# Performance work log

Measured on AMD Instinct MI355X. Metric: run time of the kernel, lower is better.

Reference implementation:

```python
import jax, jax.numpy as jnp
import numpy as np

N = 50000      # nodes
E = 800000     # edges
G = 1024       # graphs in batch
D_IN = 9       # atom feature dim
D = 64         # embedding_size


def _lin(k, fan_in, shape):
    s = 1.0 / np.sqrt(fan_in)
    return jax.random.uniform(k, shape, jnp.float32, -s, s)


def setup_inputs() -> dict:
    key = jax.random.key(0)
    ks = jax.random.split(key, 12)
    x = jax.random.normal(ks[0], (N, D_IN), dtype=jnp.float32)
    edge_index = jax.random.randint(ks[1], (2, E), 0, N, dtype=jnp.int32)
    # node -> graph id, sorted, every graph non-empty
    batch = (jnp.arange(N) * G // N).astype(jnp.int32)
    W0 = _lin(ks[2], D_IN, (D_IN, D)); b0 = _lin(ks[3], D_IN, (D,))
    W1 = _lin(ks[4], D, (D, D));       b1 = _lin(ks[5], D, (D,))
    W2 = _lin(ks[6], D, (D, D));       b2 = _lin(ks[7], D, (D,))
    W3 = _lin(ks[8], D, (D, D));       b3 = _lin(ks[9], D, (D,))
    Wout = _lin(ks[10], 2 * D, (2 * D, 1)); bout = _lin(ks[11], 2 * D, (1,))
    return {"x": x, "edge_index": edge_index, "batch": batch,
            "W0": W0, "b0": b0, "W1": W1, "b1": b1,
            "W2": W2, "b2": b2, "W3": W3, "b3": b3,
            "Wout": Wout, "bout": bout}


def reference(x, edge_index, batch, W0, b0, W1, b1, W2, b2, W3, b3, Wout, bout):
    n = x.shape[0]
    # GCNConv: add self-loops, symmetric normalization D^-1/2 (A+I) D^-1/2
    loops = jnp.arange(n, dtype=edge_index.dtype)
    row = jnp.concatenate([edge_index[0], loops])  # source
    col = jnp.concatenate([edge_index[1], loops])  # destination
    deg = jax.ops.segment_sum(jnp.ones_like(col, dtype=x.dtype), col, num_segments=n)
    dinv = jax.lax.rsqrt(deg)  # deg >= 1 thanks to self-loops
    norm = dinv[row] * dinv[col]  # [E+N]

    def conv(h, W, b):
        h = h @ W                               # [N, D]
        msg = norm[:, None] * h[row]            # [E+N, D]
        return jax.ops.segment_sum(msg, col, num_segments=n) + b

    h = jnp.tanh(conv(x, W0, b0))
    h = jnp.tanh(conv(h, W1, b1))
    h = jnp.tanh(conv(h, W2, b2))
    h = jnp.tanh(conv(h, W3, b3))
    # dropout is identity in eval mode
    gmax = jax.ops.segment_max(h, batch, num_segments=G)                       # [G, D]
    cnt = jax.ops.segment_sum(jnp.ones((n, 1), h.dtype), batch, num_segments=G)
    gmean = jax.ops.segment_sum(h, batch, num_segments=G) / jnp.maximum(cnt, 1.0)
    pooled = jnp.concatenate([gmax, gmean], axis=1)                            # [G, 2D]
    return pooled @ Wout + bout
```

## Files before the change

### kernel.cpp

```cpp
#include <hip/hip_runtime.h>
#include <hip/hip_fp16.h>
#include <math.h>

#define N_NODES 50000
#define N_EDGES 800000
#define N_GRAPHS 1024
#define DIM 64
#define PAD 64
#define ZROW N_NODES
#define SLICE 6250
#define QBLK 208


__global__ void deg_fill(const int* __restrict__ row, const int* __restrict__ col,
                         int* __restrict__ ideg, int* __restrict__ esrc_pad) {
    int slice = blockIdx.x & 7;
    int q = blockIdx.x >> 3;
    int lo = slice * SLICE, hi = lo + SLICE;
    for (int e = q * 256 + threadIdx.x; e < N_EDGES; e += QBLK * 256) {
        int c = col[e];
        if (c >= lo && c < hi) {
            int rank = atomicAdd(&ideg[c], 1);
            if (rank < PAD) esrc_pad[c * PAD + rank] = row[e];
        }
    }
}


__global__ void gemm9(const float* __restrict__ x, const float* __restrict__ W,
                      const int* __restrict__ ideg, __half* __restrict__ th) {
    __shared__ float Wl[9 * DIM];
    int tid = threadIdx.x;
    for (int i = tid; i < 9 * DIM; i += 256) Wl[i] = W[i];
    __syncthreads();
    int node = blockIdx.x * 4 + (tid >> 6);
    int d = tid & 63;
    if (node >= N_NODES) return;
    const float* xr = x + (size_t)node * 9;
    float acc = 0.0f;
#pragma unroll
    for (int k = 0; k < 9; ++k) acc += xr[k] * Wl[k * DIM + d];
    float dv = rsqrtf((float)ideg[node] + 1.0f);
    th[(size_t)node * DIM + d] = __float2half(dv * acc);
}

__global__ void gemm64(const float* __restrict__ h, const float* __restrict__ W,
                       const int* __restrict__ ideg, uint2* __restrict__ th2) {
    __shared__ float At[64][68];
    __shared__ float Bl[64][68];
    int tid = threadIdx.x;
    int n0 = blockIdx.x * 64;

    {
        const float4* W4 = (const float4*)W;
#pragma unroll
        for (int i = 0; i < 4; ++i) {
            int idx = tid + 256 * i;
            int k = idx >> 4;
            int d4 = idx & 15;
            float4 v = W4[idx];
            *(float4*)&Bl[k][d4 * 4] = v;
        }
    }
    {
        int node = tid >> 2;
        int seg = tid & 3;
        int gn = n0 + node;
        bool ok = gn < N_NODES;
        const float4* h4 = (const float4*)h;
#pragma unroll
        for (int i = 0; i < 4; ++i) {
            int c4 = seg * 4 + i;
            float4 v = ok ? h4[(size_t)gn * 16 + c4] : make_float4(0.f, 0.f, 0.f, 0.f);
            int d = c4 * 4;
            At[d + 0][node] = v.x;
            At[d + 1][node] = v.y;
            At[d + 2][node] = v.z;
            At[d + 3][node] = v.w;
        }
    }
    __syncthreads();

    int ty = tid >> 4;
    int tx = tid & 15;
    float c00 = 0, c01 = 0, c02 = 0, c03 = 0;
    float c10 = 0, c11 = 0, c12 = 0, c13 = 0;
    float c20 = 0, c21 = 0, c22 = 0, c23 = 0;
    float c30 = 0, c31 = 0, c32 = 0, c33 = 0;
#pragma unroll 8
    for (int k = 0; k < 64; ++k) {
        float4 a = *(const float4*)&At[k][ty * 4];
        float4 b = *(const float4*)&Bl[k][tx * 4];
        c00 += a.x * b.x; c01 += a.x * b.y; c02 += a.x * b.z; c03 += a.x * b.w;
        c10 += a.y * b.x; c11 += a.y * b.y; c12 += a.y * b.z; c13 += a.y * b.w;
        c20 += a.z * b.x; c21 += a.z * b.y; c22 += a.z * b.z; c23 += a.z * b.w;
        c30 += a.w * b.x; c31 += a.w * b.y; c32 += a.w * b.z; c33 += a.w * b.w;
    }
    int gn = n0 + ty * 4;
#define STORE_ROW(r, CA, CB, CC, CD)                                          \
    if (gn + r < N_NODES) {                                                   \
        float dv = rsqrtf((float)ideg[gn + r] + 1.0f);                        \
        __half2 p0 = __floats2half2_rn(dv * CA, dv * CB);                     \
        __half2 p1 = __floats2half2_rn(dv * CC, dv * CD);                     \
        uint2 o;                                                              \
        o.x = *(unsigned*)&p0;                                                \
        o.y = *(unsigned*)&p1;                                                \
        th2[(size_t)(gn + r) * 16 + tx] = o;                                  \
    }
    STORE_ROW(0, c00, c01, c02, c03)
    STORE_ROW(1, c10, c11, c12, c13)
    STORE_ROW(2, c20, c21, c22, c23)
    STORE_ROW(3, c30, c31, c32, c33)
#undef STORE_ROW
}


__device__ __forceinline__ float4 h4tof4(uint2 v) {
    __half2 a = *reinterpret_cast<const __half2*>(&v.x);
    __half2 c = *reinterpret_cast<const __half2*>(&v.y);
    float2 fa = __half22float2(a);
    float2 fc = __half22float2(c);
    return make_float4(fa.x, fa.y, fc.x, fc.y);
}

__device__ __forceinline__ void add4(float4& a, const float4& r) {
    a.x += r.x; a.y += r.y; a.z += r.z; a.w += r.w;
}

__global__ void gather_tanh(const int* __restrict__ esrc_pad, const int* __restrict__ ideg,
                            const uint2* __restrict__ th2, const float* __restrict__ b,
                            float4* __restrict__ hout4) {
    int tid = threadIdx.x;
    int wid = tid >> 6;
    int lane = tid & 63;
    int sub = lane & 15;
    int grp = lane >> 4;
    int node = blockIdx.x * 16 + wid * 4 + grp;

    int deg = min(ideg[node], PAD);
    const int* ep = esrc_pad + node * PAD;

    float4 acc0 = h4tof4(th2[(size_t)node * 16 + sub]);
    float4 acc1 = make_float4(0.f, 0.f, 0.f, 0.f);
    float4 acc2 = make_float4(0.f, 0.f, 0.f, 0.f);
    float4 acc3 = make_float4(0.f, 0.f, 0.f, 0.f);

    for (int base = 0; base < deg; base += 16) {
        int4 i0 = *(const int4*)(ep + base + 0);
        int4 i1 = *(const int4*)(ep + base + 4);
        int4 i2 = *(const int4*)(ep + base + 8);
        int4 i3 = *(const int4*)(ep + base + 12);
        int idx[16] = {i0.x, i0.y, i0.z, i0.w, i1.x, i1.y, i1.z, i1.w,
                       i2.x, i2.y, i2.z, i2.w, i3.x, i3.y, i3.z, i3.w};
        int rem = deg - base;
        uint2 r[16];
#pragma unroll
        for (int j = 0; j < 16; ++j) {
            int s = (j < rem) ? idx[j] : ZROW;
            r[j] = th2[(size_t)s * 16 + sub];
        }
#pragma unroll
        for (int j = 0; j < 16; ++j) {
            float4 v = h4tof4(r[j]);
            if ((j & 3) == 0) add4(acc0, v);
            else if ((j & 3) == 1) add4(acc1, v);
            else if ((j & 3) == 2) add4(acc2, v);
            else add4(acc3, v);
        }
    }

    float4 acc;
    acc.x = (acc0.x + acc1.x) + (acc2.x + acc3.x);
    acc.y = (acc0.y + acc1.y) + (acc2.y + acc3.y);
    acc.z = (acc0.z + acc1.z) + (acc2.z + acc3.z);
    acc.w = (acc0.w + acc1.w) + (acc2.w + acc3.w);

    float4 bv = ((const float4*)b)[sub];
    float dv = rsqrtf((float)deg + 1.0f);
    float4 res;
    res.x = tanhf(dv * acc.x + bv.x);
    res.y = tanhf(dv * acc.y + bv.y);
    res.z = tanhf(dv * acc.z + bv.z);
    res.w = tanhf(dv * acc.w + bv.w);
    hout4[(size_t)node * 16 + sub] = res;
}


__device__ __forceinline__ int lower_bound(const int* a, int n, int key) {
    int lo = 0, hi = n;
    while (lo < hi) {
        int mid = (lo + hi) >> 1;
        if (a[mid] < key) lo = mid + 1; else hi = mid;
    }
    return lo;
}

__global__ void pool_out(const float* __restrict__ h, const int* __restrict__ batch,
                         const float* __restrict__ Wout, const float* __restrict__ bout,
                         float* __restrict__ out) {
    __shared__ float smax[4][DIM];
    __shared__ float ssum[4][DIM];
    __shared__ int bounds[2];
    int g = blockIdx.x;
    int tid = threadIdx.x, w = tid >> 6, d = tid & 63;
    if (tid == 0) {
        bounds[0] = lower_bound(batch, N_NODES, g);
        bounds[1] = lower_bound(batch, N_NODES, g + 1);
    }
    __syncthreads();
    int start = bounds[0], end = bounds[1];
    float mx = -INFINITY, sum = 0.0f;
    for (int n = start + w; n < end; n += 4) {
        float v = h[(size_t)n * DIM + d];
        mx = fmaxf(mx, v);
        sum += v;
    }
    smax[w][d] = mx;
    ssum[w][d] = sum;
    __syncthreads();
    if (w == 0) {
        mx = fmaxf(fmaxf(smax[0][d], smax[1][d]), fmaxf(smax[2][d], smax[3][d]));
        sum = ssum[0][d] + ssum[1][d] + ssum[2][d] + ssum[3][d];
        float cnt = (float)(end - start);
        float mean = sum / fmaxf(cnt, 1.0f);
        float v = mx * Wout[d] + mean * Wout[DIM + d];
#pragma unroll
        for (int off = 32; off > 0; off >>= 1) v += __shfl_down(v, off, 64);
        if (d == 0) out[g] = v + bout[0];
    }
}


static inline size_t align256(size_t x) { return (x + 255) & ~(size_t)255; }

extern "C" void kernel_launch(void* const* d_in, const int* in_sizes, int n_in,
                              void* d_out, int out_size, void* d_ws, size_t ws_size,
                              hipStream_t stream) {
    const float* x     = (const float*)d_in[0];
    const int*   ei    = (const int*)d_in[1];
    const int*   batch = (const int*)d_in[2];
    const float* W0    = (const float*)d_in[3];
    const float* b0    = (const float*)d_in[4];
    const float* W1    = (const float*)d_in[5];
    const float* b1    = (const float*)d_in[6];
    const float* W2    = (const float*)d_in[7];
    const float* b2    = (const float*)d_in[8];
    const float* W3    = (const float*)d_in[9];
    const float* b3    = (const float*)d_in[10];
    const float* Wout  = (const float*)d_in[11];
    const float* bout  = (const float*)d_in[12];
    float* out = (float*)d_out;

    const int* row = ei;
    const int* col = ei + N_EDGES;

    char* ws = (char*)d_ws;
    size_t off = 0;
    int*    ideg     = (int*)(ws + off);    off += align256((size_t)N_NODES * 4);
    int*    esrc_pad = (int*)(ws + off);    off += align256((size_t)N_NODES * PAD * 4);
    __half* th       = (__half*)(ws + off); off += align256(((size_t)N_NODES + 1) * DIM * 2);
    float*  hA       = (float*)(ws + off);  off += align256((size_t)N_NODES * DIM * 4);
    (void)ws_size;

    const int wave_blocks = N_NODES / 4;
    const int gath_blocks = N_NODES / 16;
    const int gemm_blocks = (N_NODES + 63) / 64;

    hipMemsetAsync(ideg, 0, (size_t)N_NODES * 4, stream);
    hipMemsetAsync(th + (size_t)ZROW * DIM, 0, DIM * 2, stream);
    deg_fill<<<8 * QBLK, 256, 0, stream>>>(row, col, ideg, esrc_pad);

    gemm9<<<wave_blocks, 256, 0, stream>>>(x, W0, ideg, th);
    gather_tanh<<<gath_blocks, 256, 0, stream>>>(esrc_pad, ideg, (const uint2*)th, b0, (float4*)hA);

    const float* Ws[3] = {W1, W2, W3};
    const float* bs[3] = {b1, b2, b3};
    for (int l = 0; l < 3; ++l) {
        gemm64<<<gemm_blocks, 256, 0, stream>>>(hA, Ws[l], ideg, (uint2*)th);
        gather_tanh<<<gath_blocks, 256, 0, stream>>>(esrc_pad, ideg, (const uint2*)th, bs[l], (float4*)hA);
    }

    pool_out<<<N_GRAPHS, 256, 0, stream>>>(hA, batch, Wout, bout, out);
    (void)out_size; (void)n_in; (void)in_sizes;
}
```

Baseline: 274.8 us.

## Fuse all GCN layers and pooling into one cooperative persistent kernel

Replaces the sequence of gemm9, gemm64, gather_tanh and pool_out launches with a single cooperative kernel. It uses grid-stride loops over tiles and grid.sync() between phases, with a grid of up to 2 blocks per CU over 256 CUs. The goal is to cut the launch overhead and tail gaps of nine separate kernels. In exchange, occupancy is capped at 2 blocks per CU, grid-wide barriers add their own cost, and the latency-bound gather phase may lose parallelism compared with the original 3125-block launch.

```diff
diff --git a/kernel.cpp b/kernel.cpp
--- a/kernel.cpp
+++ b/kernel.cpp
@@ -1,6 +1,9 @@
 #include <hip/hip_runtime.h>
 #include <hip/hip_fp16.h>
+#include <hip/hip_cooperative_groups.h>
 #include <math.h>
+
+namespace cg = cooperative_groups;
 
 #define N_NODES 50000
 #define N_EDGES 800000
@@ -27,92 +30,13 @@
 }
 
 
-__global__ void gemm9(const float* __restrict__ x, const float* __restrict__ W,
-                      const int* __restrict__ ideg, __half* __restrict__ th) {
-    __shared__ float Wl[9 * DIM];
-    int tid = threadIdx.x;
-    for (int i = tid; i < 9 * DIM; i += 256) Wl[i] = W[i];
-    __syncthreads();
-    int node = blockIdx.x * 4 + (tid >> 6);
-    int d = tid & 63;
-    if (node >= N_NODES) return;
-    const float* xr = x + (size_t)node * 9;
-    float acc = 0.0f;
-#pragma unroll
-    for (int k = 0; k < 9; ++k) acc += xr[k] * Wl[k * DIM + d];
-    float dv = rsqrtf((float)ideg[node] + 1.0f);
-    th[(size_t)node * DIM + d] = __float2half(dv * acc);
-}
-
-__global__ void gemm64(const float* __restrict__ h, const float* __restrict__ W,
-                       const int* __restrict__ ideg, uint2* __restrict__ th2) {
-    __shared__ float At[64][68];
-    __shared__ float Bl[64][68];
-    int tid = threadIdx.x;
-    int n0 = blockIdx.x * 64;
-
-    {
-        const float4* W4 = (const float4*)W;
-#pragma unroll
-        for (int i = 0; i < 4; ++i) {
-            int idx = tid + 256 * i;
-            int k = idx >> 4;
-            int d4 = idx & 15;
-            float4 v = W4[idx];
-            *(float4*)&Bl[k][d4 * 4] = v;
-        }
-    }
-    {
-        int node = tid >> 2;
-        int seg = tid & 3;
-        int gn = n0 + node;
-        bool ok = gn < N_NODES;
-        const float4* h4 = (const float4*)h;
-#pragma unroll
-        for (int i = 0; i < 4; ++i) {
-            int c4 = seg * 4 + i;
-            float4 v = ok ? h4[(size_t)gn * 16 + c4] : make_float4(0.f, 0.f, 0.f, 0.f);
-            int d = c4 * 4;
-            At[d + 0][node] = v.x;
-            At[d + 1][node] = v.y;
-            At[d + 2][node] = v.z;
-            At[d + 3][node] = v.w;
-        }
-    }
-    __syncthreads();
-
-    int ty = tid >> 4;
-    int tx = tid & 15;
-    float c00 = 0, c01 = 0, c02 = 0, c03 = 0;
-    float c10 = 0, c11 = 0, c12 = 0, c13 = 0;
-    float c20 = 0, c21 = 0, c22 = 0, c23 = 0;
-    float c30 = 0, c31 = 0, c32 = 0, c33 = 0;
-#pragma unroll 8
-    for (int k = 0; k < 64; ++k) {
-        float4 a = *(const float4*)&At[k][ty * 4];
-        float4 b = *(const float4*)&Bl[k][tx * 4];
-        c00 += a.x * b.x; c01 += a.x * b.y; c02 += a.x * b.z; c03 += a.x * b.w;
-        c10 += a.y * b.x; c11 += a.y * b.y; c12 += a.y * b.z; c13 += a.y * b.w;
-        c20 += a.z * b.x; c21 += a.z * b.y; c22 += a.z * b.z; c23 += a.z * b.w;
-        c30 += a.w * b.x; c31 += a.w * b.y; c32 += a.w * b.z; c33 += a.w * b.w;
-    }
-    int gn = n0 + ty * 4;
-#define STORE_ROW(r, CA, CB, CC, CD)                                          \
-    if (gn + r < N_NODES) {                                                   \
-        float dv = rsqrtf((float)ideg[gn + r] + 1.0f);                        \
-        __half2 p0 = __floats2half2_rn(dv * CA, dv * CB);                     \
-        __half2 p1 = __floats2half2_rn(dv * CC, dv * CD);                     \
-        uint2 o;                                                              \
-        o.x = *(unsigned*)&p0;                                                \
-        o.y = *(unsigned*)&p1;                                                \
-        th2[(size_t)(gn + r) * 16 + tx] = o;                                  \
-    }
-    STORE_ROW(0, c00, c01, c02, c03)
-    STORE_ROW(1, c10, c11, c12, c13)
-    STORE_ROW(2, c20, c21, c22, c23)
-    STORE_ROW(3, c30, c31, c32, c33)
-#undef STORE_ROW
-}
+struct SharedMem {
+    union {
+        struct { float At[64][68]; float Bl[64][68]; } g;
+        float W9[9 * DIM];
+        struct { float smax[4][DIM]; float ssum[4][DIM]; int bounds[2]; } p;
+    };
+};
 
 
 __device__ __forceinline__ float4 h4tof4(uint2 v) {
@@ -127,106 +51,218 @@
     a.x += r.x; a.y += r.y; a.z += r.z; a.w += r.w;
 }
 
-__global__ void gather_tanh(const int* __restrict__ esrc_pad, const int* __restrict__ ideg,
-                            const uint2* __restrict__ th2, const float* __restrict__ b,
-                            float4* __restrict__ hout4) {
+__device__ __forceinline__ int lower_bound(const int* a, int n, int key) {
+    int lo = 0, hi = n;
+    while (lo < hi) {
+        int mid = (lo + hi) >> 1;
+        if (a[mid] < key) lo = mid + 1; else hi = mid;
+    }
+    return lo;
+}
+
+
+__device__ void gather_phase(const int* __restrict__ esrc_pad, const int* __restrict__ ideg,
+                             const uint2* __restrict__ th2, const float* __restrict__ b,
+                             float4* __restrict__ hout4) {
     int tid = threadIdx.x;
     int wid = tid >> 6;
     int lane = tid & 63;
     int sub = lane & 15;
     int grp = lane >> 4;
-    int node = blockIdx.x * 16 + wid * 4 + grp;
-
-    int deg = min(ideg[node], PAD);
-    const int* ep = esrc_pad + node * PAD;
-
-    float4 acc0 = h4tof4(th2[(size_t)node * 16 + sub]);
-    float4 acc1 = make_float4(0.f, 0.f, 0.f, 0.f);
-    float4 acc2 = make_float4(0.f, 0.f, 0.f, 0.f);
-    float4 acc3 = make_float4(0.f, 0.f, 0.f, 0.f);
-
-    for (int base = 0; base < deg; base += 16) {
-        int4 i0 = *(const int4*)(ep + base + 0);
-        int4 i1 = *(const int4*)(ep + base + 4);
-        int4 i2 = *(const int4*)(ep + base + 8);
-        int4 i3 = *(const int4*)(ep + base + 12);
-        int idx[16] = {i0.x, i0.y, i0.z, i0.w, i1.x, i1.y, i1.z, i1.w,
-                       i2.x, i2.y, i2.z, i2.w, i3.x, i3.y, i3.z, i3.w};
-        int rem = deg - base;
-        uint2 r[16];
-#pragma unroll
-        for (int j = 0; j < 16; ++j) {
-            int s = (j < rem) ? idx[j] : ZROW;
-            r[j] = th2[(size_t)s * 16 + sub];
-        }
-#pragma unroll
-        for (int j = 0; j < 16; ++j) {
-            float4 v = h4tof4(r[j]);
-            if ((j & 3) == 0) add4(acc0, v);
-            else if ((j & 3) == 1) add4(acc1, v);
-            else if ((j & 3) == 2) add4(acc2, v);
-            else add4(acc3, v);
-        }
-    }
-
-    float4 acc;
-    acc.x = (acc0.x + acc1.x) + (acc2.x + acc3.x);
-    acc.y = (acc0.y + acc1.y) + (acc2.y + acc3.y);
-    acc.z = (acc0.z + acc1.z) + (acc2.z + acc3.z);
-    acc.w = (acc0.w + acc1.w) + (acc2.w + acc3.w);
-
-    float4 bv = ((const float4*)b)[sub];
-    float dv = rsqrtf((float)deg + 1.0f);
-    float4 res;
-    res.x = tanhf(dv * acc.x + bv.x);
-    res.y = tanhf(dv * acc.y + bv.y);
-    res.z = tanhf(dv * acc.z + bv.z);
-    res.w = tanhf(dv * acc.w + bv.w);
-    hout4[(size_t)node * 16 + sub] = res;
-}
-
-
-__device__ __forceinline__ int lower_bound(const int* a, int n, int key) {
-    int lo = 0, hi = n;
-    while (lo < hi) {
-        int mid = (lo + hi) >> 1;
-        if (a[mid] < key) lo = mid + 1; else hi = mid;
-    }
-    return lo;
-}
-
-__global__ void pool_out(const float* __restrict__ h, const int* __restrict__ batch,
-                         const float* __restrict__ Wout, const float* __restrict__ bout,
-                         float* __restrict__ out) {
-    __shared__ float smax[4][DIM];
-    __shared__ float ssum[4][DIM];
-    __shared__ int bounds[2];
-    int g = blockIdx.x;
-    int tid = threadIdx.x, w = tid >> 6, d = tid & 63;
-    if (tid == 0) {
-        bounds[0] = lower_bound(batch, N_NODES, g);
-        bounds[1] = lower_bound(batch, N_NODES, g + 1);
+    for (int t = blockIdx.x; t < N_NODES / 16; t += gridDim.x) {
+        int node = t * 16 + wid * 4 + grp;
+        int deg = min(ideg[node], PAD);
+        const int* ep = esrc_pad + node * PAD;
+
+        float4 acc0 = h4tof4(th2[(size_t)node * 16 + sub]);
+        float4 acc1 = make_float4(0.f, 0.f, 0.f, 0.f);
+        float4 acc2 = make_float4(0.f, 0.f, 0.f, 0.f);
+        float4 acc3 = make_float4(0.f, 0.f, 0.f, 0.f);
+
+        for (int base = 0; base < deg; base += 16) {
+            int4 i0 = *(const int4*)(ep + base + 0);
+            int4 i1 = *(const int4*)(ep + base + 4);
+            int4 i2 = *(const int4*)(ep + base + 8);
+            int4 i3 = *(const int4*)(ep + base + 12);
+            int idx[16] = {i0.x, i0.y, i0.z, i0.w, i1.x, i1.y, i1.z, i1.w,
+                           i2.x, i2.y, i2.z, i2.w, i3.x, i3.y, i3.z, i3.w};
+            int rem = deg - base;
+            uint2 r[16];
+#pragma unroll
+            for (int j = 0; j < 16; ++j) {
+                int s = (j < rem) ? idx[j] : ZROW;
+                r[j] = th2[(size_t)s * 16 + sub];
+            }
+#pragma unroll
+            for (int j = 0; j < 16; ++j) {
+                float4 v = h4tof4(r[j]);
+                if ((j & 3) == 0) add4(acc0, v);
+                else if ((j & 3) == 1) add4(acc1, v);
+                else if ((j & 3) == 2) add4(acc2, v);
+                else add4(acc3, v);
+            }
+        }
+
+        float4 acc;
+        acc.x = (acc0.x + acc1.x) + (acc2.x + acc3.x);
+        acc.y = (acc0.y + acc1.y) + (acc2.y + acc3.y);
+        acc.z = (acc0.z + acc1.z) + (acc2.z + acc3.z);
+        acc.w = (acc0.w + acc1.w) + (acc2.w + acc3.w);
+
+        float4 bv = ((const float4*)b)[sub];
+        float dv = rsqrtf((float)deg + 1.0f);
+        float4 res;
+        res.x = tanhf(dv * acc.x + bv.x);
+        res.y = tanhf(dv * acc.y + bv.y);
+        res.z = tanhf(dv * acc.z + bv.z);
+        res.w = tanhf(dv * acc.w + bv.w);
+        hout4[(size_t)node * 16 + sub] = res;
+    }
+}
+
+__device__ void gemm64_phase(SharedMem* sh, const float* __restrict__ h,
+                             const float* __restrict__ W, const int* __restrict__ ideg,
+                             uint2* __restrict__ th2) {
+    int tid = threadIdx.x;
+    {
+        const float4* W4 = (const float4*)W;
+#pragma unroll
+        for (int i = 0; i < 4; ++i) {
+            int idx = tid + 256 * i;
+            int k = idx >> 4;
+            int d4 = idx & 15;
+            *(float4*)&sh->g.Bl[k][d4 * 4] = W4[idx];
+        }
     }
     __syncthreads();
-    int start = bounds[0], end = bounds[1];
-    float mx = -INFINITY, sum = 0.0f;
-    for (int n = start + w; n < end; n += 4) {
-        float v = h[(size_t)n * DIM + d];
-        mx = fmaxf(mx, v);
-        sum += v;
-    }
-    smax[w][d] = mx;
-    ssum[w][d] = sum;
+    int ty = tid >> 4;
+    int tx = tid & 15;
+    for (int t = blockIdx.x; t < (N_NODES + 63) / 64; t += gridDim.x) {
+        int n0 = t * 64;
+        {
+            int node = tid >> 2;
+            int seg = tid & 3;
+            int gn = n0 + node;
+            bool ok = gn < N_NODES;
+            const float4* h4 = (const float4*)h;
+#pragma unroll
+            for (int i = 0; i < 4; ++i) {
+                int c4 = seg * 4 + i;
+                float4 v = ok ? h4[(size_t)gn * 16 + c4] : make_float4(0.f, 0.f, 0.f, 0.f);
+                int d = c4 * 4;
+                sh->g.At[d + 0][node] = v.x;
+                sh->g.At[d + 1][node] = v.y;
+                sh->g.At[d + 2][node] = v.z;
+                sh->g.At[d + 3][node] = v.w;
+            }
+        }
+        __syncthreads();
+
+        float c00 = 0, c01 = 0, c02 = 0, c03 = 0;
+        float c10 = 0, c11 = 0, c12 = 0, c13 = 0;
+        float c20 = 0, c21 = 0, c22 = 0, c23 = 0;
+        float c30 = 0, c31 = 0, c32 = 0, c33 = 0;
+#pragma unroll 8
+        for (int k = 0; k < 64; ++k) {
+            float4 a = *(const float4*)&sh->g.At[k][ty * 4];
+            float4 b = *(const float4*)&sh->g.Bl[k][tx * 4];
+            c00 += a.x * b.x; c01 += a.x * b.y; c02 += a.x * b.z; c03 += a.x * b.w;
+            c10 += a.y * b.x; c11 += a.y * b.y; c12 += a.y * b.z; c13 += a.y * b.w;
+            c20 += a.z * b.x; c21 += a.z * b.y; c22 += a.z * b.z; c23 += a.z * b.w;
+            c30 += a.w * b.x; c31 += a.w * b.y; c32 += a.w * b.z; c33 += a.w * b.w;
+        }
+        int gn = n0 + ty * 4;
+#define STORE_ROW(r, CA, CB, CC, CD)                                          \
+        if (gn + r < N_NODES) {                                               \
+            float dv = rsqrtf((float)ideg[gn + r] + 1.0f);                    \
+            __half2 p0 = __floats2half2_rn(dv * CA, dv * CB);                 \
+            __half2 p1 = __floats2half2_rn(dv * CC, dv * CD);                 \
+            uint2 o;                                                          \
+            o.x = *(unsigned*)&p0;                                            \
+            o.y = *(unsigned*)&p1;                                            \
+            th2[(size_t)(gn + r) * 16 + tx] = o;                              \
+        }
+        STORE_ROW(0, c00, c01, c02, c03)
+        STORE_ROW(1, c10, c11, c12, c13)
+        STORE_ROW(2, c20, c21, c22, c23)
+        STORE_ROW(3, c30, c31, c32, c33)
+#undef STORE_ROW
+        __syncthreads();
+    }
+}
+
+
+__global__ __launch_bounds__(256, 2) void mega(
+    const float* __restrict__ x,
+    const float* __restrict__ W0, const float* __restrict__ b0,
+    const float* __restrict__ W1, const float* __restrict__ b1,
+    const float* __restrict__ W2, const float* __restrict__ b2,
+    const float* __restrict__ W3, const float* __restrict__ b3,
+    const float* __restrict__ Wout, const float* __restrict__ bout,
+    const int* __restrict__ batch,
+    const int* __restrict__ ideg, const int* __restrict__ esrc_pad,
+    __half* __restrict__ th, float* __restrict__ hA,
+    float* __restrict__ out)
+{
+    cg::grid_group grid = cg::this_grid();
+    __shared__ SharedMem sh;
+    int tid = threadIdx.x;
+
+    for (int i = tid; i < 9 * DIM; i += 256) sh.W9[i] = W0[i];
     __syncthreads();
-    if (w == 0) {
-        mx = fmaxf(fmaxf(smax[0][d], smax[1][d]), fmaxf(smax[2][d], smax[3][d]));
-        sum = ssum[0][d] + ssum[1][d] + ssum[2][d] + ssum[3][d];
-        float cnt = (float)(end - start);
-        float mean = sum / fmaxf(cnt, 1.0f);
-        float v = mx * Wout[d] + mean * Wout[DIM + d];
-#pragma unroll
-        for (int off = 32; off > 0; off >>= 1) v += __shfl_down(v, off, 64);
-        if (d == 0) out[g] = v + bout[0];
+    for (int t = blockIdx.x; t < N_NODES / 4; t += gridDim.x) {
+        int node = t * 4 + (tid >> 6);
+        int d = tid & 63;
+        const float* xr = x + (size_t)node * 9;
+        float acc = 0.f;
+#pragma unroll
+        for (int k = 0; k < 9; ++k) acc += xr[k] * sh.W9[k * DIM + d];
+        float dv = rsqrtf((float)ideg[node] + 1.0f);
+        th[(size_t)node * DIM + d] = __float2half(dv * acc);
+    }
+    grid.sync();
+
+    gather_phase(esrc_pad, ideg, (const uint2*)th, b0, (float4*)hA);
+    grid.sync();
+
+    const float* Ws[3] = {W1, W2, W3};
+    const float* bs[3] = {b1, b2, b3};
+    for (int l = 0; l < 3; ++l) {
+        gemm64_phase(&sh, hA, Ws[l], ideg, (uint2*)th);
+        grid.sync();
+        gather_phase(esrc_pad, ideg, (const uint2*)th, bs[l], (float4*)hA);
+        grid.sync();
+    }
+
+    for (int g = blockIdx.x; g < N_GRAPHS; g += gridDim.x) {
+        int w = tid >> 6, d = tid & 63;
+        if (tid == 0) {
+            sh.p.bounds[0] = lower_bound(batch, N_NODES, g);
+            sh.p.bounds[1] = lower_bound(batch, N_NODES, g + 1);
+        }
+        __syncthreads();
+        int start = sh.p.bounds[0], end = sh.p.bounds[1];
+        float mx = -INFINITY, sum = 0.0f;
+        for (int n = start + w; n < end; n += 4) {
+            float v = hA[(size_t)n * DIM + d];
+            mx = fmaxf(mx, v);
+            sum += v;
+        }
+        sh.p.smax[w][d] = mx;
+        sh.p.ssum[w][d] = sum;
+        __syncthreads();
+        if (w == 0) {
+            mx = fmaxf(fmaxf(sh.p.smax[0][d], sh.p.smax[1][d]),
+                       fmaxf(sh.p.smax[2][d], sh.p.smax[3][d]));
+            sum = sh.p.ssum[0][d] + sh.p.ssum[1][d] + sh.p.ssum[2][d] + sh.p.ssum[3][d];
+            float cnt = (float)(end - start);
+            float mean = sum / fmaxf(cnt, 1.0f);
+            float v = mx * Wout[d] + mean * Wout[DIM + d];
+#pragma unroll
+            for (int off2 = 32; off2 > 0; off2 >>= 1) v += __shfl_down(v, off2, 64);
+            if (d == 0) out[g] = v + bout[0];
+        }
+        __syncthreads();
     }
 }
 
@@ -262,24 +298,24 @@
     float*  hA       = (float*)(ws + off);  off += align256((size_t)N_NODES * DIM * 4);
     (void)ws_size;
 
-    const int wave_blocks = N_NODES / 4;
-    const int gath_blocks = N_NODES / 16;
-    const int gemm_blocks = (N_NODES + 63) / 64;
-
     hipMemsetAsync(ideg, 0, (size_t)N_NODES * 4, stream);
     hipMemsetAsync(th + (size_t)ZROW * DIM, 0, DIM * 2, stream);
     deg_fill<<<8 * QBLK, 256, 0, stream>>>(row, col, ideg, esrc_pad);
 
-    gemm9<<<wave_blocks, 256, 0, stream>>>(x, W0, ideg, th);
-    gather_tanh<<<gath_blocks, 256, 0, stream>>>(esrc_pad, ideg, (const uint2*)th, b0, (float4*)hA);
-
-    const float* Ws[3] = {W1, W2, W3};
-    const float* bs[3] = {b1, b2, b3};
-    for (int l = 0; l < 3; ++l) {
-        gemm64<<<gemm_blocks, 256, 0, stream>>>(hA, Ws[l], ideg, (uint2*)th);
-        gather_tanh<<<gath_blocks, 256, 0, stream>>>(esrc_pad, ideg, (const uint2*)th, bs[l], (float4*)hA);
-    }
-
-    pool_out<<<N_GRAPHS, 256, 0, stream>>>(hA, batch, Wout, bout, out);
+    static int blocks_per_cu = -1;
+    if (blocks_per_cu < 0) {
+        int occ = 0;
+        hipOccupancyMaxActiveBlocksPerMultiprocessor(&occ, (const void*)mega, 256, 0);
+        blocks_per_cu = occ < 1 ? 1 : (occ > 2 ? 2 : occ);
+    }
+    int mblocks = blocks_per_cu * 256;
+
+    void* args[] = {(void*)&x,
+                    (void*)&W0, (void*)&b0, (void*)&W1, (void*)&b1,
+                    (void*)&W2, (void*)&b2, (void*)&W3, (void*)&b3,
+                    (void*)&Wout, (void*)&bout, (void*)&batch,
+                    (void*)&ideg, (void*)&esrc_pad, (void*)&th, (void*)&hA,
+                    (void*)&out};
+    hipLaunchCooperativeKernel((void*)mega, dim3(mblocks), dim3(256), args, 0, stream);
     (void)out_size; (void)n_in; (void)in_sizes;
 }
```

Result: slower. 760.3 us (+176.7%).
